# Kernel tuning notes

Hardware: AMD Instinct MI355X
Metric: run time of the kernel (lower is better)

The kernel has to match this reference:

```python
import jax, jax.numpy as jnp
import numpy as np

B, S, H, D = 2, 2048, 16, 64


def setup_inputs() -> dict:
    key = jax.random.key(0)
    kq, kk, kv, km = jax.random.split(key, 4)
    q = jax.random.normal(kq, (B, S, H, D), dtype=jnp.float32)
    k = jax.random.normal(kk, (B, S, H, D), dtype=jnp.float32)
    v = jax.random.normal(kv, (B, S, H, D), dtype=jnp.float32)
    pattern_mask = jax.random.bernoulli(km, 0.1, (S, S))
    return {"q": q, "k": k, "v": v, "pattern_mask": pattern_mask}


def reference(q, k, v, pattern_mask):
    # Faithful math of the torch module: for each query row i, attend only to
    # columns j where pattern_mask[i, j]; softmax over the selected columns
    # per (batch, head); rows with no selected columns produce zeros.
    head_dim = q.shape[-1]
    scale = 1.0 / jnp.sqrt(jnp.asarray(head_dim, dtype=q.dtype))
    # scores: [B, H, S_q, S_k]
    scores = jnp.einsum('bihd,bjhd->bhij', q, k) * scale
    neg = jnp.finfo(scores.dtype).min
    masked = jnp.where(pattern_mask[None, None, :, :], scores, neg)
    attn = jax.nn.softmax(masked, axis=-1)
    # zero out rows with no active columns (softmax over all-masked row is uniform garbage)
    row_has = jnp.any(pattern_mask, axis=-1)  # [S]
    attn = jnp.where(row_has[None, None, :, None], attn, jnp.zeros((), dtype=attn.dtype))
    # output: [B, S, H, D]
    out = jnp.einsum('bhij,bjhd->bihd', attn, v)
    return out
```

## Files before the change

### kernel.cpp

```cpp
#include <hip/hip_runtime.h>
#include <hip/hip_bf16.h>
#include <math.h>

#define SLEN 2048
#define NBATCH 2
#define NH 16
#define DH 64
#define WPR 64
#define NROUND 32
#define IMGB 8192
#define CONVBLK (NBATCH * NH * NROUND)
#define PACKBLK (SLEN * WPR / 256)

typedef __attribute__((ext_vector_type(4))) short short4v;
typedef __attribute__((ext_vector_type(8))) short short8v;
typedef __attribute__((ext_vector_type(4))) float float4v;

typedef __attribute__((address_space(1))) void gas_void;
typedef __attribute__((address_space(3))) void las_void;

__device__ __forceinline__ unsigned short f2bf(float f) {
  unsigned u = __float_as_uint(f);
  u += 0x7fffu + ((u >> 16) & 1u);
  return (unsigned short)(u >> 16);
}

__device__ __forceinline__ float fexp2(float x) {
#if __has_builtin(__builtin_amdgcn_exp2f)
  return __builtin_amdgcn_exp2f(x);
#else
  return __expf(x * 0.6931471805599453f);
#endif
}

__device__ __forceinline__ unsigned pack_bf2(float a, float b) {
  unsigned ua = __float_as_uint(a); ua += 0x7fffu + ((ua >> 16) & 1u);
  unsigned ub = __float_as_uint(b); ub += 0x7fffu + ((ub >> 16) & 1u);
  return __builtin_amdgcn_perm(ub, ua, 0x07060302u);
}

__device__ __forceinline__ unsigned cvtpk(float lo, float hi) {
  unsigned r;
  asm("v_cvt_pk_bf16_f32 %0, %1, %2" : "=v"(r) : "v"(lo), "v"(hi));
  return r;
}

__global__ void detect_layout_kernel(const uint4* __restrict__ m,
                                     int* __restrict__ flag) {
  const int tid = threadIdx.x;
  unsigned a0 = 0, amid = 0;
#pragma unroll
  for (int i = 0; i < 16; i++) {
    uint4 x = m[tid + i * 256];
    unsigned w = (x.x | x.y) | (x.z | x.w);
    a0 |= w & 0x000000ffu;
    amid |= w & 0xffffff00u;
  }
  __shared__ int s0, sm;
  if (tid == 0) { s0 = 0; sm = 0; }
  __syncthreads();
  const int lane0 = ((tid & 63) == 0);
  if (__any(a0 != 0) && lane0) atomicOr(&s0, 1);
  if (__any(amid != 0) && lane0) atomicOr(&sm, 1);
  __syncthreads();
  if (tid == 0) flag[0] = (s0 && sm) ? 1 : 0;
}

__device__ __forceinline__ unsigned nib4(unsigned w) {
  return ((w * 0x01020408u) >> 24) & 0xFu;
}

__device__ __forceinline__ int kperm(int kp) {
  return (kp & 0x23) | ((kp >> 1) & 0x0C) | ((kp << 2) & 0x10);
}

__global__ __launch_bounds__(256) void prep_kernel(
    const float* __restrict__ kk, const float* __restrict__ vv,
    const void* __restrict__ mask, const int* __restrict__ flag,
    char* __restrict__ kb, char* __restrict__ vb,
    unsigned* __restrict__ packed) {
  const int tid = threadIdx.x;
  if (blockIdx.x >= CONVBLK) {
    const int w = (blockIdx.x - CONVBLK) * 256 + tid;
    unsigned bits = 0u;
    if (*flag) {
      const uint4* mp = (const uint4*)((const char*)mask + (size_t)w * 32);
      uint4 x = mp[0], y = mp[1];
      bits = nib4(x.x) | (nib4(x.y) << 4) | (nib4(x.z) << 8) | (nib4(x.w) << 12) |
             (nib4(y.x) << 16) | (nib4(y.y) << 20) | (nib4(y.z) << 24) | (nib4(y.w) << 28);
    } else {
      const unsigned* m = (const unsigned*)mask + (size_t)w * 32;
#pragma unroll
      for (int j = 0; j < 32; j++) bits |= (m[j] ? 1u : 0u) << j;
    }
    packed[w] = bits;
    return;
  }
  const int bid = blockIdx.x;
  const int t = bid & 31;
  const int bh = bid >> 5;
  const int b = bh >> 4, h = bh & 15;
  char* kimg = kb + (size_t)bid * IMGB;
  char* vimg = vb + (size_t)bid * IMGB;

  {
    const int r = tid >> 2;
    const int dg = (tid & 3) << 4;
    const float* src = kk + (((size_t)(b * SLEN + t * 64 + r) * NH + h) * DH + dg);
    const int rimg = kperm(r);
    char* rowp = kimg + rimg * 128;
    const int swz = (rimg & 7) << 4;
#pragma unroll
    for (int i = 0; i < 4; i++) {
      float4v x = *(const float4v*)(src + i * 4);
      const int d0 = dg + i * 4;
      const int off = (d0 * 2) ^ swz;
      union { unsigned u[2]; short4v s4; } cv;
      cv.u[0] = pack_bf2(x.x, x.y);
      cv.u[1] = pack_bf2(x.z, x.w);
      *(short4v*)(rowp + off) = cv.s4;
    }
  }
  {
    const int d = tid >> 2;
    const int kg = (tid & 3) << 4;
    char* rowp = vimg + d * 128;
    const int swz = (d & 7) << 4;
    const float* src = vv + ((size_t)(b * SLEN + t * 64 + kg) * NH + h) * DH + d;
#pragma unroll
    for (int i = 0; i < 16; i++) {
      const int c = kg + i;
      float x = src[(size_t)i * (NH * DH)];
      const int off = (c * 2) ^ swz;
      *(unsigned short*)(rowp + off) = f2bf(x);
    }
  }
}

__global__ __launch_bounds__(256, 4) void sattn_fast5(
    const float* __restrict__ q, const unsigned* __restrict__ pmask,
    const char* __restrict__ kb, const char* __restrict__ vb,
    float* __restrict__ out) {
  __shared__ __align__(16) char Kbuf[2][IMGB];
  __shared__ __align__(16) char Vbuf[2][IMGB];

  const int tid = threadIdx.x;
  const int xcd = blockIdx.x & 7;
  const int j = blockIdx.x >> 3;
  const int bh = xcd * 4 + (j >> 5);
  const int chunk = j & 31;
  const int b = bh >> 4;
  const int h = bh & 15;
  const int wave = tid >> 6;
  const int lane = tid & 63;
  const int lq = lane & 15;
  const int g = lane >> 4;
  const int swz = (lq & 7) << 4;
  const int g8 = g << 3;
  const int g16 = g << 4;

  const int qrow = chunk * 64 + wave * 16 + lq;
  const int qw = qrow * WPR;

  const float SCL2 = 0.18033688011112042f;
  short8v qf[2];
  {
    const float* qp = q + (((size_t)b * SLEN + qrow) * NH + h) * DH;
#pragma unroll
    for (int ds = 0; ds < 2; ds++) {
      float4v x0 = *(const float4v*)(qp + ds * 32 + g8);
      float4v x1 = *(const float4v*)(qp + ds * 32 + g8 + 4);
      union { unsigned u[4]; short8v s8; } cv;
      cv.u[0] = pack_bf2(x0.x * SCL2, x0.y * SCL2);
      cv.u[1] = pack_bf2(x0.z * SCL2, x0.w * SCL2);
      cv.u[2] = pack_bf2(x1.x * SCL2, x1.y * SCL2);
      cv.u[3] = pack_bf2(x1.z * SCL2, x1.w * SCL2);
      qf[ds] = cv.s8;
    }
  }

  short8v ones;
#pragma unroll
  for (int i = 0; i < 8; i++) ones[i] = (short)0x3F80;

  const char* gK = kb + (size_t)bh * (NROUND * IMGB) + tid * 16;
  const char* gV = vb + (size_t)bh * (NROUND * IMGB) + tid * 16;

  float4v acc[4] = {};
  float4v lacc = {};

  uint2 m = *(const uint2*)&pmask[qw];

  {
    char* lK = &Kbuf[0][0] + tid * 16;
    char* lV = &Vbuf[0][0] + tid * 16;
#pragma unroll
    for (int i = 0; i < 2; i++) {
      __builtin_amdgcn_global_load_lds((gas_void*)(gK + i * 4096), (las_void*)(lK + i * 4096), 16, 0, 0);
      __builtin_amdgcn_global_load_lds((gas_void*)(gV + i * 4096), (las_void*)(lV + i * 4096), 16, 0, 0);
    }
  }
  __syncthreads();

  for (int t = 0; t < NROUND; t++) {
    const int bt = t & 1;
    const unsigned m0 = m.x, m1 = m.y;
    if (t + 1 < NROUND) {
      m = *(const uint2*)&pmask[qw + 2 * (t + 1)];
      const char* nK = gK + (size_t)(t + 1) * IMGB;
      const char* nV = gV + (size_t)(t + 1) * IMGB;
      char* lK = &Kbuf[bt ^ 1][0] + tid * 16;
      char* lV = &Vbuf[bt ^ 1][0] + tid * 16;
#pragma unroll
      for (int i = 0; i < 2; i++) {
        __builtin_amdgcn_global_load_lds((gas_void*)(nK + i * 4096), (las_void*)(lK + i * 4096), 16, 0, 0);
        __builtin_amdgcn_global_load_lds((gas_void*)(nV + i * 4096), (las_void*)(lV + i * 4096), 16, 0, 0);
      }
    }

    const char* Kl = &Kbuf[bt][0];
    float4v st[4];
#pragma unroll
    for (int s = 0; s < 4; s++) {
      const char* rowp = Kl + (s * 16 + lq) * 128;
      short8v kf0 = *(const short8v*)(rowp + ((g16) ^ swz));
      short8v kf1 = *(const short8v*)(rowp + ((64 + g16) ^ swz));
      float4v z = {0.f, 0.f, 0.f, 0.f};
      z = __builtin_amdgcn_mfma_f32_16x16x32_bf16(kf0, qf[0], z, 0, 0, 0);
      z = __builtin_amdgcn_mfma_f32_16x16x32_bf16(kf1, qf[1], z, 0, 0, 0);
      st[s] = z;
    }

    float pv[4][4];
#pragma unroll
    for (int s = 0; s < 4; s++) {
      const int sh = g8 + ((s & 1) << 2);
      const unsigned hw = ((s < 2) ? m0 : m1) >> sh;
      float p0 = fexp2(st[s][0]); p0 = (hw & 1u) ? p0 : 0.f;
      float p1 = fexp2(st[s][1]); p1 = (hw & 2u) ? p1 : 0.f;
      float p2 = fexp2(st[s][2]); p2 = (hw & 4u) ? p2 : 0.f;
      float p3 = fexp2(st[s][3]); p3 = (hw & 8u) ? p3 : 0.f;
      pv[s][0] = p0; pv[s][1] = p1; pv[s][2] = p2; pv[s][3] = p3;
    }
    short8v pf[2];
#pragma unroll
    for (int kt = 0; kt < 2; kt++) {
      union { unsigned u[4]; short8v s8; } pa;
      pa.u[0] = cvtpk(pv[2 * kt][0], pv[2 * kt][1]);
      pa.u[1] = cvtpk(pv[2 * kt][2], pv[2 * kt][3]);
      pa.u[2] = cvtpk(pv[2 * kt + 1][0], pv[2 * kt + 1][1]);
      pa.u[3] = cvtpk(pv[2 * kt + 1][2], pv[2 * kt + 1][3]);
      pf[kt] = pa.s8;
    }

    const char* Vl = &Vbuf[bt][0];
    lacc = __builtin_amdgcn_mfma_f32_16x16x32_bf16(ones, pf[0], lacc, 0, 0, 0);
    lacc = __builtin_amdgcn_mfma_f32_16x16x32_bf16(ones, pf[1], lacc, 0, 0, 0);
#pragma unroll
    for (int n = 0; n < 4; n++) {
      const char* rowp = Vl + (n * 16 + lq) * 128;
      short8v vf0 = *(const short8v*)(rowp + ((g16) ^ swz));
      short8v vf1 = *(const short8v*)(rowp + ((64 + g16) ^ swz));
      float4v a = acc[n];
      a = __builtin_amdgcn_mfma_f32_16x16x32_bf16(vf0, pf[0], a, 0, 0, 0);
      a = __builtin_amdgcn_mfma_f32_16x16x32_bf16(vf1, pf[1], a, 0, 0, 0);
      acc[n] = a;
    }
    __syncthreads();
  }

  const float l = lacc[0];
  const float inv = (l > 0.f) ? 1.f / l : 0.f;
  float* op = out + (((size_t)b * SLEN + qrow) * NH + h) * DH;
#pragma unroll
  for (int n = 0; n < 4; n++) {
    float4v o;
    o.x = acc[n][0] * inv; o.y = acc[n][1] * inv;
    o.z = acc[n][2] * inv; o.w = acc[n][3] * inv;
    *(float4v*)(op + n * 16 + g * 4) = o;
  }
}

__global__ __launch_bounds__(256) void sattn_fallback(
    const float* __restrict__ q, const float* __restrict__ kk,
    const float* __restrict__ vv, const unsigned int* __restrict__ pmask,
    float* __restrict__ out) {
  __shared__ __align__(16) unsigned short Kt[16 * 64];
  __shared__ __align__(16) unsigned short Vt[64 * 20];

  const int tid = threadIdx.x;
  const int chunk = blockIdx.x & 31;
  const int bh = blockIdx.x >> 5;
  const int b = bh >> 4;
  const int h = bh & 15;
  const int wave = tid >> 6;
  const int lane = tid & 63;
  const int lq = lane & 15;
  const int g = lane >> 4;

  const int qrow = chunk * 64 + wave * 16 + lq;

  short4v qf[4];
  {
    const float* qp = q + (((size_t)b * SLEN + qrow) * NH + h) * DH;
#pragma unroll
    for (int ks = 0; ks < 4; ks++) {
      float4v x = *(const float4v*)(qp + ks * 16 + g * 4);
      short4v s;
      s.x = (short)f2bf(x.x); s.y = (short)f2bf(x.y);
      s.z = (short)f2bf(x.z); s.w = (short)f2bf(x.w);
      qf[ks] = s;
    }
  }

  const int srow = tid >> 4;
  const int scol = (tid & 15) * 4;
  const size_t kvbase = (size_t)b * SLEN * (NH * DH) + (size_t)h * DH;

  float4v acc[4] = {};
  float m_run = -INFINITY;
  float l_run = 0.f;

  for (int t = 0; t < SLEN / 16; t++) {
    const int kbase = t * 16;
    __syncthreads();
    {
      const size_t rowoff = kvbase + (size_t)(kbase + srow) * (NH * DH) + scol;
      float4v x = *(const float4v*)(kk + rowoff);
      short4v s;
      s.x = (short)f2bf(x.x); s.y = (short)f2bf(x.y);
      s.z = (short)f2bf(x.z); s.w = (short)f2bf(x.w);
      const int off = (scol * 2) ^ ((srow & 7) << 4);
      *(short4v*)((char*)Kt + srow * 128 + off) = s;

      float4v y = *(const float4v*)(vv + rowoff);
      Vt[(scol + 0) * 20 + srow] = f2bf(y.x);
      Vt[(scol + 1) * 20 + srow] = f2bf(y.y);
      Vt[(scol + 2) * 20 + srow] = f2bf(y.z);
      Vt[(scol + 3) * 20 + srow] = f2bf(y.w);
    }
    __syncthreads();

    float4v stv = {0.f, 0.f, 0.f, 0.f};
#pragma unroll
    for (int ks = 0; ks < 4; ks++) {
      const int off = ((ks * 16 + g * 4) * 2) ^ ((lq & 7) << 4);
      short4v kf = *(const short4v*)((const char*)Kt + lq * 128 + off);
      stv = __builtin_amdgcn_mfma_f32_16x16x16bf16_1k(kf, qf[ks], stv, 0, 0, 0);
    }

    const unsigned int mw = pmask[qrow * WPR + (kbase >> 5)];
    const int shift = (kbase & 16) + g * 4;
    float sc[4];
    float tmax = -INFINITY;
#pragma unroll
    for (int r = 0; r < 4; r++) {
      bool a = (mw >> (shift + r)) & 1u;
      sc[r] = a ? stv[r] * 0.125f : -INFINITY;
      tmax = fmaxf(tmax, sc[r]);
    }
    tmax = fmaxf(tmax, __shfl_xor(tmax, 16));
    tmax = fmaxf(tmax, __shfl_xor(tmax, 32));
    const float mnew = fmaxf(m_run, tmax);
    const float muse = (mnew > -1e37f) ? mnew : 0.f;
    const float alpha = __expf(m_run - muse);
    float p[4], tsum = 0.f;
#pragma unroll
    for (int r = 0; r < 4; r++) {
      p[r] = __expf(sc[r] - muse);
      tsum += p[r];
    }
    tsum += __shfl_xor(tsum, 16);
    tsum += __shfl_xor(tsum, 32);
    l_run = l_run * alpha + tsum;
    m_run = mnew;

    short4v pfv;
    pfv.x = (short)f2bf(p[0]); pfv.y = (short)f2bf(p[1]);
    pfv.z = (short)f2bf(p[2]); pfv.w = (short)f2bf(p[3]);

#pragma unroll
    for (int n = 0; n < 4; n++) {
      acc[n][0] *= alpha; acc[n][1] *= alpha;
      acc[n][2] *= alpha; acc[n][3] *= alpha;
      short4v vf = *(const short4v*)((const char*)Vt + ((n * 16 + lq) * 20 + g * 4) * 2);
      acc[n] = __builtin_amdgcn_mfma_f32_16x16x16bf16_1k(vf, pfv, acc[n], 0, 0, 0);
    }
  }

  const float inv = (l_run > 0.f) ? 1.f / l_run : 0.f;
  float* op = out + (((size_t)b * SLEN + qrow) * NH + h) * DH;
#pragma unroll
  for (int n = 0; n < 4; n++) {
    float4v o;
    o.x = acc[n][0] * inv; o.y = acc[n][1] * inv;
    o.z = acc[n][2] * inv; o.w = acc[n][3] * inv;
    *(float4v*)(op + n * 16 + g * 4) = o;
  }
}

extern "C" void kernel_launch(void* const* d_in, const int* in_sizes, int n_in,
                              void* d_out, int out_size, void* d_ws, size_t ws_size,
                              hipStream_t stream) {
  const float* q = (const float*)d_in[0];
  const float* k = (const float*)d_in[1];
  const float* v = (const float*)d_in[2];
  const void* mask = d_in[3];
  float* out = (float*)d_out;

  int* flag = (int*)d_ws;
  unsigned int* packed = (unsigned int*)((char*)d_ws + 256);
  char* kb = (char*)d_ws + (1 << 20);
  char* vb = kb + (size_t)NBATCH * NH * NROUND * IMGB;
  const size_t need = (size_t)(1 << 20) + 2 * (size_t)NBATCH * NH * NROUND * IMGB;

  detect_layout_kernel<<<1, 256, 0, stream>>>((const uint4*)mask, flag);

  if (ws_size >= need) {
    prep_kernel<<<CONVBLK + PACKBLK, 256, 0, stream>>>(k, v, mask, flag, kb, vb, packed);
    sattn_fast5<<<NBATCH * NH * (SLEN / 64), 256, 0, stream>>>(q, packed, kb, vb, out);
  } else {
    prep_kernel<<<CONVBLK + PACKBLK, 256, 0, stream>>>(k, v, mask, flag, kb, vb, packed);
    sattn_fallback<<<NBATCH * NH * (SLEN / 64), 256, 0, stream>>>(q, k, v, packed, out);
  }
}
```

Before: 82.24 us.

## Fold mask layout detection into prep kernel, hoist V loads, add MFMA priority

Removes the separate single-block layout-detection launch. Each packing block now works out bool-vs-int32 mask layout from its own 32-byte slice using a block-wide OR. In the attention kernel, the V fragments are loaded from LDS before the softmax/exp work so their latency overlaps ALU work, and s_setprio raises wave priority around the MFMA sections. Per-block detection could disagree with the former global decision on sparse or unusual masks, and hoisting the V fragments raises register pressure.

```diff
diff --git a/kernel.cpp b/kernel.cpp
--- a/kernel.cpp
+++ b/kernel.cpp
@@ -45,27 +45,6 @@
   return r;
 }
 
-__global__ void detect_layout_kernel(const uint4* __restrict__ m,
-                                     int* __restrict__ flag) {
-  const int tid = threadIdx.x;
-  unsigned a0 = 0, amid = 0;
-#pragma unroll
-  for (int i = 0; i < 16; i++) {
-    uint4 x = m[tid + i * 256];
-    unsigned w = (x.x | x.y) | (x.z | x.w);
-    a0 |= w & 0x000000ffu;
-    amid |= w & 0xffffff00u;
-  }
-  __shared__ int s0, sm;
-  if (tid == 0) { s0 = 0; sm = 0; }
-  __syncthreads();
-  const int lane0 = ((tid & 63) == 0);
-  if (__any(a0 != 0) && lane0) atomicOr(&s0, 1);
-  if (__any(amid != 0) && lane0) atomicOr(&sm, 1);
-  __syncthreads();
-  if (tid == 0) flag[0] = (s0 && sm) ? 1 : 0;
-}
-
 __device__ __forceinline__ unsigned nib4(unsigned w) {
   return ((w * 0x01020408u) >> 24) & 0xFu;
 }
@@ -76,20 +55,29 @@
 
 __global__ __launch_bounds__(256) void prep_kernel(
     const float* __restrict__ kk, const float* __restrict__ vv,
-    const void* __restrict__ mask, const int* __restrict__ flag,
+    const void* __restrict__ mask,
     char* __restrict__ kb, char* __restrict__ vb,
     unsigned* __restrict__ packed) {
   const int tid = threadIdx.x;
   if (blockIdx.x >= CONVBLK) {
     const int w = (blockIdx.x - CONVBLK) * 256 + tid;
-    unsigned bits = 0u;
-    if (*flag) {
-      const uint4* mp = (const uint4*)((const char*)mask + (size_t)w * 32);
-      uint4 x = mp[0], y = mp[1];
+    const uint4* bp = (const uint4*)((const char*)mask + (size_t)w * 32);
+    uint4 x = bp[0], y = bp[1];
+    const unsigned orw = (x.x | x.y) | (x.z | x.w) | (y.x | y.y) | (y.z | y.w);
+    __shared__ int s0, sm;
+    if (tid == 0) { s0 = 0; sm = 0; }
+    __syncthreads();
+    const int lane0 = ((tid & 63) == 0);
+    if (__any((orw & 0x000000ffu) != 0) && lane0) atomicOr(&s0, 1);
+    if (__any((orw & 0xffffff00u) != 0) && lane0) atomicOr(&sm, 1);
+    __syncthreads();
+    unsigned bits;
+    if (s0 && sm) {
       bits = nib4(x.x) | (nib4(x.y) << 4) | (nib4(x.z) << 8) | (nib4(x.w) << 12) |
              (nib4(y.x) << 16) | (nib4(y.y) << 20) | (nib4(y.z) << 24) | (nib4(y.w) << 28);
     } else {
       const unsigned* m = (const unsigned*)mask + (size_t)w * 32;
+      bits = 0u;
 #pragma unroll
       for (int j = 0; j < 32; j++) bits |= (m[j] ? 1u : 0u) << j;
     }
@@ -137,7 +125,7 @@
   }
 }
 
-__global__ __launch_bounds__(256, 4) void sattn_fast5(
+__global__ __launch_bounds__(256, 4) void sattn_fast6(
     const float* __restrict__ q, const unsigned* __restrict__ pmask,
     const char* __restrict__ kb, const char* __restrict__ vb,
     float* __restrict__ out) {
@@ -220,6 +208,7 @@
 
     const char* Kl = &Kbuf[bt][0];
     float4v st[4];
+    __builtin_amdgcn_s_setprio(1);
 #pragma unroll
     for (int s = 0; s < 4; s++) {
       const char* rowp = Kl + (s * 16 + lq) * 128;
@@ -230,6 +219,16 @@
       z = __builtin_amdgcn_mfma_f32_16x16x32_bf16(kf1, qf[1], z, 0, 0, 0);
       st[s] = z;
     }
+    __builtin_amdgcn_s_setprio(0);
+
+    const char* Vl = &Vbuf[bt][0];
+    short8v vf[4][2];
+#pragma unroll
+    for (int n = 0; n < 4; n++) {
+      const char* rowp = Vl + (n * 16 + lq) * 128;
+      vf[n][0] = *(const short8v*)(rowp + ((g16) ^ swz));
+      vf[n][1] = *(const short8v*)(rowp + ((64 + g16) ^ swz));
+    }
 
     float pv[4][4];
 #pragma unroll
@@ -253,19 +252,17 @@
       pf[kt] = pa.s8;
     }
 
-    const char* Vl = &Vbuf[bt][0];
+    __builtin_amdgcn_s_setprio(1);
     lacc = __builtin_amdgcn_mfma_f32_16x16x32_bf16(ones, pf[0], lacc, 0, 0, 0);
     lacc = __builtin_amdgcn_mfma_f32_16x16x32_bf16(ones, pf[1], lacc, 0, 0, 0);
 #pragma unroll
     for (int n = 0; n < 4; n++) {
-      const char* rowp = Vl + (n * 16 + lq) * 128;
-      short8v vf0 = *(const short8v*)(rowp + ((g16) ^ swz));
-      short8v vf1 = *(const short8v*)(rowp + ((64 + g16) ^ swz));
       float4v a = acc[n];
-      a = __builtin_amdgcn_mfma_f32_16x16x32_bf16(vf0, pf[0], a, 0, 0, 0);
-      a = __builtin_amdgcn_mfma_f32_16x16x32_bf16(vf1, pf[1], a, 0, 0, 0);
+      a = __builtin_amdgcn_mfma_f32_16x16x32_bf16(vf[n][0], pf[0], a, 0, 0, 0);
+      a = __builtin_amdgcn_mfma_f32_16x16x32_bf16(vf[n][1], pf[1], a, 0, 0, 0);
       acc[n] = a;
     }
+    __builtin_amdgcn_s_setprio(0);
     __syncthreads();
   }
 
@@ -408,19 +405,15 @@
   const void* mask = d_in[3];
   float* out = (float*)d_out;
 
-  int* flag = (int*)d_ws;
   unsigned int* packed = (unsigned int*)((char*)d_ws + 256);
   char* kb = (char*)d_ws + (1 << 20);
   char* vb = kb + (size_t)NBATCH * NH * NROUND * IMGB;
   const size_t need = (size_t)(1 << 20) + 2 * (size_t)NBATCH * NH * NROUND * IMGB;
 
-  detect_layout_kernel<<<1, 256, 0, stream>>>((const uint4*)mask, flag);
-
+  prep_kernel<<<CONVBLK + PACKBLK, 256, 0, stream>>>(k, v, mask, kb, vb, packed);
   if (ws_size >= need) {
-    prep_kernel<<<CONVBLK + PACKBLK, 256, 0, stream>>>(k, v, mask, flag, kb, vb, packed);
-    sattn_fast5<<<NBATCH * NH * (SLEN / 64), 256, 0, stream>>>(q, packed, kb, vb, out);
+    sattn_fast6<<<NBATCH * NH * (SLEN / 64), 256, 0, stream>>>(q, packed, kb, vb, out);
   } else {
-    prep_kernel<<<CONVBLK + PACKBLK, 256, 0, stream>>>(k, v, mask, flag, kb, vb, packed);
     sattn_fallback<<<NBATCH * NH * (SLEN / 64), 256, 0, stream>>>(q, k, v, packed, out);
   }
 }
```

After: 77.04 us. -6.3%, faster.
